# Kernel tuning notes

Hardware: AMD Instinct MI355X
Metric: run time of the kernel (lower is better)

The kernel has to match this reference:

```python
import jax, jax.numpy as jnp
import numpy as np

B, C, H, W = 32, 256, 32, 32   # C == embedding_dim
K = 1024                        # num_embeddings
COMMITMENT_COST = 1.5
NU = 0.0


def setup_inputs() -> dict:
    key = jax.random.key(0)
    k1, k2, k3 = jax.random.split(key, 3)
    inputs = jax.random.normal(k1, (B, C, H, W), dtype=jnp.float32)
    embedding = jax.random.normal(k2, (K, C), dtype=jnp.float32)
    u = jax.random.uniform(k3, (B * H * W, K), dtype=jnp.float32,
                           minval=1e-20, maxval=1.0)
    gumbel = -jnp.log(-jnp.log(u))  # standard Gumbel(0,1) noise
    return {"inputs": inputs, "embedding": embedding, "gumbel": gumbel}


def reference(inputs, embedding, gumbel):
    # NCHW -> NHWC, flatten spatial/batch dims
    x = jnp.transpose(inputs, (0, 2, 3, 1))            # [B,H,W,D]
    shp = x.shape
    flat = x.reshape(-1, shp[-1])                      # [N,D]

    # squared-L2 distances to codebook: [N,K]
    d = (jnp.sum(flat * flat, axis=1, keepdims=True)
         + jnp.sum(embedding * embedding, axis=1)
         - 2.0 * (flat @ embedding.T))

    # gumbel_softmax(-d, tau=1, hard=True) with straight-through estimator
    y_soft = jax.nn.softmax(-d + gumbel, axis=-1)
    idx = jnp.argmax(y_soft, axis=-1)
    y_hard = jax.nn.one_hot(idx, embedding.shape[0], dtype=y_soft.dtype)
    encodings = y_hard + y_soft - jax.lax.stop_gradient(y_soft)  # [N,K]

    quantized = (encodings @ embedding).reshape(shp)   # [B,H,W,D]

    # losses
    e_latent_loss = jnp.mean((jax.lax.stop_gradient(quantized) - x) ** 2)
    probs = jax.nn.sigmoid(-d)
    kld_discrete = jnp.mean(jnp.sum(probs * jnp.log(jnp.clip(probs, 1e-8)), axis=-1))
    loss = COMMITMENT_COST * (
        kld_discrete
        + e_latent_loss * jax.lax.stop_gradient(
            kld_discrete / jnp.clip(e_latent_loss, 1e-8)))

    quantized = quantized + NU * (quantized - jax.lax.stop_gradient(quantized))

    avg_probs = jnp.mean(encodings, axis=0)
    perplexity = jnp.exp(-jnp.sum(avg_probs * jnp.log(avg_probs + 1e-10)))

    return (loss, jnp.transpose(quantized, (0, 3, 1, 2)), perplexity, encodings)
```

## Files before the change

kernel.cpp:

```cpp
#include <hip/hip_runtime.h>
#include <math.h>

#define NROWS 32768
#define KCODES 1024
#define DDIM 256
#define BM 32
#define QUANT_OFF 1
#define PERP_OFF  8388609
#define ENC_OFF   8388610
#define EPACK_OFF 4096


typedef _Float16 f16x8 __attribute__((ext_vector_type(8)));
typedef float    f32x16 __attribute__((ext_vector_type(16)));

__global__ void __launch_bounds__(256)
vq_setup(const float* __restrict__ emb, float* __restrict__ ws) {
    int k = blockIdx.x * 256 + threadIdx.x;
    if (k < KCODES) {
        const float* row = emb + (size_t)k * DDIM;
        float s = 0.f;
        #pragma unroll 4
        for (int c = 0; c < DDIM; c += 4) {
            float4 v = *(const float4*)(row + c);
            s = fmaf(v.x, v.x, s); s = fmaf(v.y, v.y, s);
            s = fmaf(v.z, v.z, s); s = fmaf(v.w, v.w, s);
        }
        ws[k] = s;
        ws[KCODES + k] = 0.f;
        if (k == 0) { ws[2 * KCODES] = 0.f; ws[2 * KCODES + 1] = 0.f; }
    }
}

__global__ void __launch_bounds__(256)
vq_pack(const float* __restrict__ emb, float* __restrict__ ws) {
    int u = blockIdx.x * 256 + threadIdx.x;
    int n    = u & 1023;
    int kg   = (u >> 10) & 1;
    int ks   = (u >> 11) & 15;
    int part = (u >> 15) & 1;
    int d0 = ks * 16 + kg * 8;
    const float* src = emb + (size_t)n * DDIM + d0;
    float4 v0 = *(const float4*)(src);
    float4 v1 = *(const float4*)(src + 4);
    float x[8] = {v0.x, v0.y, v0.z, v0.w, v1.x, v1.y, v1.z, v1.w};
    union { _Float16 h[8]; uint4 q; } p;
    #pragma unroll
    for (int j = 0; j < 8; ++j) {
        _Float16 hh = (_Float16)x[j];
        p.h[j] = part ? (_Float16)(x[j] - (float)hh) : hh;
    }
    ((uint4*)(ws + EPACK_OFF))[u] = p.q;
}

__global__ void __launch_bounds__(256, 3)
vq_main(const float* __restrict__ inp, const float* __restrict__ emb,
        const float* __restrict__ gmb, float* __restrict__ out,
        float* __restrict__ ws) {
    __shared__ uint4 apack[2048];
    __shared__ float xchunk[64][33];
    __shared__ float xn2p[8][BM];
    __shared__ float xn2[BM];
    __shared__ float rrv[BM][4];
    __shared__ int   rri[BM][4];
    __shared__ int   idxs[BM];
    __shared__ float redK[4], redE[4];

    const int tid  = threadIdx.x;
    const int lane = tid & 63;
    const int wv   = tid >> 6;
    const int lrow = lane & 31;
    const int lkg  = lane >> 5;
    const int n0   = blockIdx.x * BM;
    const int b    = n0 >> 10;
    const int s0   = n0 & 1023;

    const float* e2     = ws;
    float*       counts = ws + KCODES;
    const f16x8* ep     = (const f16x8*)(ws + EPACK_OFF);

    const int crow = tid & 31;
    const int ckg  = (tid >> 5) & 1;
    const int cksl = tid >> 6;
    float xsq = 0.f;
    const float* xbase = inp + (((size_t)b * DDIM) << 10) + s0;

    #pragma unroll 1
    for (int cb = 0; cb < 4; ++cb) {
        #pragma unroll
        for (int t0 = 0; t0 < 8; ++t0) {
            int t = tid + t0 * 256;
            int r = t & 31, dd = t >> 5;
            xchunk[dd][r] = xbase[(((size_t)(cb * 64 + dd)) << 10) + r];
        }
        __syncthreads();
        {
            union { _Float16 h[8]; uint4 q; } ph, pl;
            #pragma unroll
            for (int j = 0; j < 8; ++j) {
                float x = xchunk[cksl * 16 + ckg * 8 + j][crow];
                xsq = fmaf(x, x, xsq);
                _Float16 hh = (_Float16)x;
                ph.h[j] = hh;
                pl.h[j] = (_Float16)(x - (float)hh);
            }
            int ks = cb * 4 + cksl;
            apack[(ks * 2 + ckg) * 32 + crow]        = ph.q;
            apack[((16 + ks) * 2 + ckg) * 32 + crow] = pl.q;
        }
        __syncthreads();
    }
    xn2p[tid >> 5][crow] = xsq;
    __syncthreads();
    if (tid < BM) {
        float s = 0.f;
        #pragma unroll
        for (int p = 0; p < 8; ++p) s += xn2p[p][tid];
        xn2[tid] = s;
    }
    __syncthreads();

    float rv[16]; int ri[16];
    #pragma unroll
    for (int reg = 0; reg < 16; ++reg) { rv[reg] = -1e30f; ri[reg] = 0; }
    float kld_acc = 0.f;

    #pragma unroll 1
    for (int np = 0; np < 4; ++np) {
        const int c0 = wv * 256 + np * 64 + lrow;
        const float* gb = gmb + ((size_t)n0 << 10) + c0;

        float g0r[16];
        #pragma unroll
        for (int reg = 0; reg < 16; ++reg) {
            int row = (reg & 3) + 8 * (reg >> 2) + 4 * lkg;
            g0r[reg] = gb[(size_t)row << 10];
        }

        f32x16 acc0, acc1;
        #pragma unroll
        for (int e = 0; e < 16; ++e) { acc0[e] = 0.f; acc1[e] = 0.f; }

        const f16x8* bp = ep + (size_t)(lkg * 1024 + c0);
        f16x8 Bh0 = bp[0], Bh1 = bp[32], Bl0 = bp[32768], Bl1 = bp[32768 + 32];

        #pragma unroll 2
        for (int ks = 0; ks < 16; ++ks) {
            f16x8 ah = *(const f16x8*)&apack[(ks * 2 + lkg) * 32 + lrow];
            f16x8 al = *(const f16x8*)&apack[((16 + ks) * 2 + lkg) * 32 + lrow];
            const f16x8* nb = bp + (size_t)(((ks + 1) & 15) * 2048);
            f16x8 nh0 = nb[0], nh1 = nb[32], nl0 = nb[32768], nl1 = nb[32768 + 32];
            acc0 = __builtin_amdgcn_mfma_f32_32x32x16_f16(ah, Bh0, acc0, 0, 0, 0);
            acc1 = __builtin_amdgcn_mfma_f32_32x32x16_f16(ah, Bh1, acc1, 0, 0, 0);
            acc0 = __builtin_amdgcn_mfma_f32_32x32x16_f16(ah, Bl0, acc0, 0, 0, 0);
            acc1 = __builtin_amdgcn_mfma_f32_32x32x16_f16(ah, Bl1, acc1, 0, 0, 0);
            acc0 = __builtin_amdgcn_mfma_f32_32x32x16_f16(al, Bh0, acc0, 0, 0, 0);
            acc1 = __builtin_amdgcn_mfma_f32_32x32x16_f16(al, Bh1, acc1, 0, 0, 0);
            Bh0 = nh0; Bh1 = nh1; Bl0 = nl0; Bl1 = nl1;
        }

        float g1r[16];
        #pragma unroll
        for (int reg = 0; reg < 16; ++reg) {
            int row = (reg & 3) + 8 * (reg >> 2) + 4 * lkg;
            g1r[reg] = gb[((size_t)row << 10) + 32];
        }

        {
            const float e2c = e2[c0];
            #pragma unroll
            for (int reg = 0; reg < 16; ++reg) {
                int row = (reg & 3) + 8 * (reg >> 2) + 4 * lkg;
                float dist = xn2[row] + e2c - 2.f * acc0[reg];
                float val  = g0r[reg] - dist;
                if (val > rv[reg]) { rv[reg] = val; ri[reg] = c0; }
                float p = 1.f / (1.f + __expf(dist));
                kld_acc += p * __logf(fmaxf(p, 1e-8f));
            }
        }
        {
            const float e2c = e2[c0 + 32];
            #pragma unroll
            for (int reg = 0; reg < 16; ++reg) {
                int row = (reg & 3) + 8 * (reg >> 2) + 4 * lkg;
                float dist = xn2[row] + e2c - 2.f * acc1[reg];
                float val  = g1r[reg] - dist;
                if (val > rv[reg]) { rv[reg] = val; ri[reg] = c0 + 32; }
                float p = 1.f / (1.f + __expf(dist));
                kld_acc += p * __logf(fmaxf(p, 1e-8f));
            }
        }
    }

    #pragma unroll
    for (int reg = 0; reg < 16; ++reg) {
        float v = rv[reg];
        int   c = ri[reg];
        #pragma unroll
        for (int off = 16; off > 0; off >>= 1) {
            float ov = __shfl_xor(v, off, 64);
            int   oc = __shfl_xor(c, off, 64);
            if (ov > v || (ov == v && oc < c)) { v = ov; c = oc; }
        }
        if (lrow == 0) {
            int row = (reg & 3) + 8 * (reg >> 2) + 4 * lkg;
            rrv[row][wv] = v;
            rri[row][wv] = c;
        }
    }
    __syncthreads();
    if (tid < BM) {
        float bv = rrv[tid][0]; int bc = rri[tid][0];
        #pragma unroll
        for (int w = 1; w < 4; ++w) {
            float v = rrv[tid][w]; int c = rri[tid][w];
            if (v > bv || (v == bv && c < bc)) { bv = v; bc = c; }
        }
        idxs[tid] = bc;
        atomicAdd(&counts[bc], 1.0f);
    }
    __syncthreads();

    {
        float* enc = out + ENC_OFF;
        for (int t = tid; t < BM * (KCODES / 4); t += 256) {
            int c4 = t & 255, row = t >> 8;
            int base = c4 * 4;
            int id = idxs[row];
            float4 v;
            v.x = (base + 0 == id) ? 1.f : 0.f;
            v.y = (base + 1 == id) ? 1.f : 0.f;
            v.z = (base + 2 == id) ? 1.f : 0.f;
            v.w = (base + 3 == id) ? 1.f : 0.f;
            *(float4*)(enc + ((size_t)(n0 + row) << 10) + base) = v;
        }
    }

    float elat_acc = 0.f;
    {
        float* outq = out + QUANT_OFF;
        for (int t = tid; t < DDIM * (BM / 4); t += 256) {
            int r4 = t & 7, c = t >> 3;
            float4 xv = *(const float4*)(inp + (((size_t)(b * DDIM + c)) << 10) + s0 + r4 * 4);
            float q0 = emb[(size_t)idxs[r4 * 4 + 0] * DDIM + c];
            float q1 = emb[(size_t)idxs[r4 * 4 + 1] * DDIM + c];
            float q2 = emb[(size_t)idxs[r4 * 4 + 2] * DDIM + c];
            float q3 = emb[(size_t)idxs[r4 * 4 + 3] * DDIM + c];
            float d0 = q0 - xv.x, d1 = q1 - xv.y, d2 = q2 - xv.z, d3 = q3 - xv.w;
            elat_acc = fmaf(d0, d0, elat_acc);
            elat_acc = fmaf(d1, d1, elat_acc);
            elat_acc = fmaf(d2, d2, elat_acc);
            elat_acc = fmaf(d3, d3, elat_acc);
            float4 qv = make_float4(q0, q1, q2, q3);
            *(float4*)(outq + (((size_t)(b * DDIM + c)) << 10) + s0 + r4 * 4) = qv;
        }
    }

    #pragma unroll
    for (int off = 32; off > 0; off >>= 1) {
        kld_acc  += __shfl_xor(kld_acc, off);
        elat_acc += __shfl_xor(elat_acc, off);
    }
    if ((tid & 63) == 0) { redK[wv] = kld_acc; redE[wv] = elat_acc; }
    __syncthreads();
    if (tid == 0) {
        atomicAdd(&ws[2 * KCODES],     redK[0] + redK[1] + redK[2] + redK[3]);
        atomicAdd(&ws[2 * KCODES + 1], redE[0] + redE[1] + redE[2] + redE[3]);
    }
}

__global__ void __launch_bounds__(256)
vq_finalize(const float* __restrict__ ws, float* __restrict__ out) {
    __shared__ float red[4];
    int tid = threadIdx.x;
    float s = 0.f;
    for (int k = tid; k < KCODES; k += 256) {
        float avg = ws[KCODES + k] * (1.f / (float)NROWS);
        s += avg * logf(avg + 1e-10f);
    }
    #pragma unroll
    for (int off = 32; off > 0; off >>= 1) s += __shfl_xor(s, off);
    if ((tid & 63) == 0) red[tid >> 6] = s;
    __syncthreads();
    if (tid == 0) {
        float ssum = red[0] + red[1] + red[2] + red[3];
        float perp = expf(-ssum);
        float kld  = ws[2 * KCODES]     / (float)NROWS;
        float elat = ws[2 * KCODES + 1] / (float)(NROWS * DDIM);
        float ratio = kld / fmaxf(elat, 1e-8f);
        float loss  = 1.5f * (kld + elat * ratio);
        out[0]        = loss;
        out[PERP_OFF] = perp;
    }
}

extern "C" void kernel_launch(void* const* d_in, const int* in_sizes, int n_in,
                              void* d_out, int out_size, void* d_ws, size_t ws_size,
                              hipStream_t stream) {
    const float* inp = (const float*)d_in[0];
    const float* emb = (const float*)d_in[1];
    const float* gmb = (const float*)d_in[2];
    float* out = (float*)d_out;
    float* ws  = (float*)d_ws;

    vq_setup<<<dim3(KCODES / 256), dim3(256), 0, stream>>>(emb, ws);
    vq_pack<<<dim3(256), dim3(256), 0, stream>>>(emb, ws);
    vq_main<<<dim3(NROWS / BM), dim3(256), 0, stream>>>(inp, emb, gmb, out, ws);
    vq_finalize<<<dim3(1), dim3(256), 0, stream>>>(ws, out);
}
```

Baseline: 402.2 us.

## Double-buffer codebook fragments, prefetch gumbel early, and raise occupancy to four blocks

Restructures the main distance loop. Codebook B fragments are double-buffered two k-steps ahead in a fully unrolled loop, and the gumbel noise and e2 values for the next column pass are prefetched before the current pass's reductions, so global latency overlaps MFMA work and the epilogue. The argmax is now reduced per pass through shared memory instead of holding 16 running registers, and the activation packing uses smaller 32-row chunks with the hi and lo halves split across thread halves. Launch bounds go from 3 to 4 blocks per CU, and the sigmoid-KLD term is skipped when the distance is at least 30. Risks include register pressure or spills under the tighter occupancy bound, and a small numerical change from dropping the tiny KLD terms.

Result: slower. 605.1 us (+50.5%).

```diff
diff --git a/kernel.cpp b/kernel.cpp
--- a/kernel.cpp
+++ b/kernel.cpp
@@ -53,13 +53,30 @@
     ((uint4*)(ws + EPACK_OFF))[u] = p.q;
 }
 
-__global__ void __launch_bounds__(256, 3)
+#define LOADB(SET, BASE) do { \
+    const f16x8* nb_ = (BASE); \
+    Bq[SET][0] = nb_[0];     Bq[SET][1] = nb_[32]; \
+    Bq[SET][2] = nb_[32768]; Bq[SET][3] = nb_[32768 + 32]; \
+} while (0)
+
+#define LOADG(C0) do { \
+    const float* gb_ = gmb + ((size_t)n0 << 10) + (C0); \
+    _Pragma("unroll") \
+    for (int reg_ = 0; reg_ < 16; ++reg_) { \
+        int row_ = (reg_ & 3) + 8 * (reg_ >> 2) + 4 * lkg; \
+        g0r[reg_] = gb_[(size_t)row_ << 10]; \
+        g1r[reg_] = gb_[((size_t)row_ << 10) + 32]; \
+    } \
+    e20 = e2[(C0)]; e21 = e2[(C0) + 32]; \
+} while (0)
+
+__global__ void __launch_bounds__(256, 4)
 vq_main(const float* __restrict__ inp, const float* __restrict__ emb,
         const float* __restrict__ gmb, float* __restrict__ out,
         float* __restrict__ ws) {
     __shared__ uint4 apack[2048];
-    __shared__ float xchunk[64][33];
-    __shared__ float xn2p[8][BM];
+    __shared__ float xchunk[32][33];
+    __shared__ float xn2p[4][BM];
     __shared__ float xn2[BM];
     __shared__ float rrv[BM][4];
     __shared__ int   rri[BM][4];
@@ -79,135 +96,126 @@
     float*       counts = ws + KCODES;
     const f16x8* ep     = (const f16x8*)(ws + EPACK_OFF);
 
-    const int crow = tid & 31;
-    const int ckg  = (tid >> 5) & 1;
-    const int cksl = tid >> 6;
-    float xsq = 0.f;
-    const float* xbase = inp + (((size_t)b * DDIM) << 10) + s0;
-
-    #pragma unroll 1
-    for (int cb = 0; cb < 4; ++cb) {
-        #pragma unroll
-        for (int t0 = 0; t0 < 8; ++t0) {
-            int t = tid + t0 * 256;
-            int r = t & 31, dd = t >> 5;
-            xchunk[dd][r] = xbase[(((size_t)(cb * 64 + dd)) << 10) + r];
-        }
-        __syncthreads();
-        {
-            union { _Float16 h[8]; uint4 q; } ph, pl;
+    float g0r[16], g1r[16], e20, e21;
+    LOADG(wv * 256 + lrow);
+
+    if (lane < 32) { rrv[lane][wv] = -1e30f; rri[lane][wv] = 0; }
+
+    {
+        const int crow = tid & 31;
+        const int ckg  = (tid >> 5) & 1;
+        const int cksl = (tid >> 6) & 1;
+        const int part = tid >> 7;
+        float xsq = 0.f;
+        const float* xbase = inp + (((size_t)b * DDIM) << 10) + s0;
+
+        #pragma unroll 1
+        for (int cb = 0; cb < 8; ++cb) {
             #pragma unroll
-            for (int j = 0; j < 8; ++j) {
-                float x = xchunk[cksl * 16 + ckg * 8 + j][crow];
-                xsq = fmaf(x, x, xsq);
-                _Float16 hh = (_Float16)x;
-                ph.h[j] = hh;
-                pl.h[j] = (_Float16)(x - (float)hh);
+            for (int t0 = 0; t0 < 4; ++t0) {
+                int idx = tid + t0 * 256;
+                int r = idx & 31, dd = idx >> 5;
+                xchunk[dd][r] = xbase[(((size_t)(cb * 32 + dd)) << 10) + r];
             }
-            int ks = cb * 4 + cksl;
-            apack[(ks * 2 + ckg) * 32 + crow]        = ph.q;
-            apack[((16 + ks) * 2 + ckg) * 32 + crow] = pl.q;
-        }
-        __syncthreads();
-    }
-    xn2p[tid >> 5][crow] = xsq;
+            __syncthreads();
+            {
+                const int ks = cb * 2 + cksl;
+                union { _Float16 h[8]; uint4 q; } pq;
+                #pragma unroll
+                for (int j = 0; j < 8; ++j) {
+                    float x = xchunk[cksl * 16 + ckg * 8 + j][crow];
+                    _Float16 hh = (_Float16)x;
+                    if (part == 0) { xsq = fmaf(x, x, xsq); pq.h[j] = hh; }
+                    else           { pq.h[j] = (_Float16)(x - (float)hh); }
+                }
+                if (part == 0) apack[(ks * 2 + ckg) * 32 + crow]        = pq.q;
+                else           apack[((16 + ks) * 2 + ckg) * 32 + crow] = pq.q;
+            }
+            __syncthreads();
+        }
+        if (part == 0) xn2p[(tid >> 5) & 3][crow] = xsq;
+    }
     __syncthreads();
     if (tid < BM) {
         float s = 0.f;
         #pragma unroll
-        for (int p = 0; p < 8; ++p) s += xn2p[p][tid];
+        for (int p = 0; p < 4; ++p) s += xn2p[p][tid];
         xn2[tid] = s;
     }
     __syncthreads();
 
-    float rv[16]; int ri[16];
-    #pragma unroll
-    for (int reg = 0; reg < 16; ++reg) { rv[reg] = -1e30f; ri[reg] = 0; }
+    f16x8 Bq[2][4];
+    {
+        const f16x8* bp0 = ep + (size_t)(lkg * 1024 + wv * 256 + lrow);
+        LOADB(0, bp0);
+        LOADB(1, bp0 + 2048);
+    }
+
     float kld_acc = 0.f;
 
     #pragma unroll 1
     for (int np = 0; np < 4; ++np) {
         const int c0 = wv * 256 + np * 64 + lrow;
-        const float* gb = gmb + ((size_t)n0 << 10) + c0;
-
-        float g0r[16];
-        #pragma unroll
-        for (int reg = 0; reg < 16; ++reg) {
-            int row = (reg & 3) + 8 * (reg >> 2) + 4 * lkg;
-            g0r[reg] = gb[(size_t)row << 10];
-        }
+        const f16x8* bpn = ep + (size_t)(lkg * 1024 + c0);
 
         f32x16 acc0, acc1;
         #pragma unroll
         for (int e = 0; e < 16; ++e) { acc0[e] = 0.f; acc1[e] = 0.f; }
 
-        const f16x8* bp = ep + (size_t)(lkg * 1024 + c0);
-        f16x8 Bh0 = bp[0], Bh1 = bp[32], Bl0 = bp[32768], Bl1 = bp[32768 + 32];
-
-        #pragma unroll 2
+        #pragma unroll
         for (int ks = 0; ks < 16; ++ks) {
+            const int cur = ks & 1;
             f16x8 ah = *(const f16x8*)&apack[(ks * 2 + lkg) * 32 + lrow];
             f16x8 al = *(const f16x8*)&apack[((16 + ks) * 2 + lkg) * 32 + lrow];
-            const f16x8* nb = bp + (size_t)(((ks + 1) & 15) * 2048);
-            f16x8 nh0 = nb[0], nh1 = nb[32], nl0 = nb[32768], nl1 = nb[32768 + 32];
-            acc0 = __builtin_amdgcn_mfma_f32_32x32x16_f16(ah, Bh0, acc0, 0, 0, 0);
-            acc1 = __builtin_amdgcn_mfma_f32_32x32x16_f16(ah, Bh1, acc1, 0, 0, 0);
-            acc0 = __builtin_amdgcn_mfma_f32_32x32x16_f16(ah, Bl0, acc0, 0, 0, 0);
-            acc1 = __builtin_amdgcn_mfma_f32_32x32x16_f16(ah, Bl1, acc1, 0, 0, 0);
-            acc0 = __builtin_amdgcn_mfma_f32_32x32x16_f16(al, Bh0, acc0, 0, 0, 0);
-            acc1 = __builtin_amdgcn_mfma_f32_32x32x16_f16(al, Bh1, acc1, 0, 0, 0);
-            Bh0 = nh0; Bh1 = nh1; Bl0 = nl0; Bl1 = nl1;
-        }
-
-        float g1r[16];
+            acc0 = __builtin_amdgcn_mfma_f32_32x32x16_f16(ah, Bq[cur][0], acc0, 0, 0, 0);
+            acc1 = __builtin_amdgcn_mfma_f32_32x32x16_f16(ah, Bq[cur][1], acc1, 0, 0, 0);
+            acc0 = __builtin_amdgcn_mfma_f32_32x32x16_f16(ah, Bq[cur][2], acc0, 0, 0, 0);
+            acc1 = __builtin_amdgcn_mfma_f32_32x32x16_f16(ah, Bq[cur][3], acc1, 0, 0, 0);
+            acc0 = __builtin_amdgcn_mfma_f32_32x32x16_f16(al, Bq[cur][0], acc0, 0, 0, 0);
+            acc1 = __builtin_amdgcn_mfma_f32_32x32x16_f16(al, Bq[cur][1], acc1, 0, 0, 0);
+            if (ks < 14) LOADB(cur, bpn + (size_t)((ks + 2) * 2048));
+        }
+
+        float vbest[16]; int cbest[16];
         #pragma unroll
         for (int reg = 0; reg < 16; ++reg) {
-            int row = (reg & 3) + 8 * (reg >> 2) + 4 * lkg;
-            g1r[reg] = gb[((size_t)row << 10) + 32];
-        }
-
-        {
-            const float e2c = e2[c0];
+            const int row = (reg & 3) + 8 * (reg >> 2) + 4 * lkg;
+            const float xnr = xn2[row];
+            float d0 = xnr + e20 - 2.f * acc0[reg];
+            float d1 = xnr + e21 - 2.f * acc1[reg];
+            float v0 = g0r[reg] - d0;
+            float v1 = g1r[reg] - d1;
+            if (d0 < 30.f) { float p = 1.f / (1.f + __expf(d0)); kld_acc += p * __logf(fmaxf(p, 1e-8f)); }
+            if (d1 < 30.f) { float p = 1.f / (1.f + __expf(d1)); kld_acc += p * __logf(fmaxf(p, 1e-8f)); }
+            if (v1 > v0) { vbest[reg] = v1; cbest[reg] = c0 + 32; }
+            else         { vbest[reg] = v0; cbest[reg] = c0; }
+        }
+
+        if (np < 3) {
+            const f16x8* bp2 = bpn + 64;
+            LOADB(0, bp2);
+            LOADB(1, bp2 + 2048);
+            LOADG(c0 + 64);
+        }
+
+        #pragma unroll
+        for (int reg = 0; reg < 16; ++reg) {
+            float v = vbest[reg];
+            int   c = cbest[reg];
             #pragma unroll
-            for (int reg = 0; reg < 16; ++reg) {
-                int row = (reg & 3) + 8 * (reg >> 2) + 4 * lkg;
-                float dist = xn2[row] + e2c - 2.f * acc0[reg];
-                float val  = g0r[reg] - dist;
-                if (val > rv[reg]) { rv[reg] = val; ri[reg] = c0; }
-                float p = 1.f / (1.f + __expf(dist));
-                kld_acc += p * __logf(fmaxf(p, 1e-8f));
+            for (int off = 16; off > 0; off >>= 1) {
+                float ov = __shfl_xor(v, off, 32);
+                int   oc = __shfl_xor(c, off, 32);
+                if (ov > v || (ov == v && oc < c)) { v = ov; c = oc; }
             }
-        }
-        {
-            const float e2c = e2[c0 + 32];
-            #pragma unroll
-            for (int reg = 0; reg < 16; ++reg) {
-                int row = (reg & 3) + 8 * (reg >> 2) + 4 * lkg;
-                float dist = xn2[row] + e2c - 2.f * acc1[reg];
-                float val  = g1r[reg] - dist;
-                if (val > rv[reg]) { rv[reg] = val; ri[reg] = c0 + 32; }
-                float p = 1.f / (1.f + __expf(dist));
-                kld_acc += p * __logf(fmaxf(p, 1e-8f));
+            if (lrow == 0) {
+                const int row = (reg & 3) + 8 * (reg >> 2) + 4 * lkg;
+                float pv = rrv[row][wv]; int pc = rri[row][wv];
+                if (v > pv || (v == pv && c < pc)) { rrv[row][wv] = v; rri[row][wv] = c; }
             }
         }
     }
 
-    #pragma unroll
-    for (int reg = 0; reg < 16; ++reg) {
-        float v = rv[reg];
-        int   c = ri[reg];
-        #pragma unroll
-        for (int off = 16; off > 0; off >>= 1) {
-            float ov = __shfl_xor(v, off, 64);
-            int   oc = __shfl_xor(c, off, 64);
-            if (ov > v || (ov == v && oc < c)) { v = ov; c = oc; }
-        }
-        if (lrow == 0) {
-            int row = (reg & 3) + 8 * (reg >> 2) + 4 * lkg;
-            rrv[row][wv] = v;
-            rri[row][wv] = c;
-        }
-    }
     __syncthreads();
     if (tid < BM) {
         float bv = rrv[tid][0]; int bc = rri[tid][0];
```
